# Kernel tuning notes

Hardware: AMD Instinct MI355X
Metric: run time of the kernel (lower is better)

The kernel has to match this reference:

```python
import jax, jax.numpy as jnp
import numpy as np
import math

B, N, D, H = 16, 200, 2048, 2048  # batch, seq (== max_len), feature dim, hidden/output dim


def setup_inputs() -> dict:
    key = jax.random.key(0)
    ks = jax.random.split(key, 16)
    s = 1.0 / math.sqrt(D)
    return {
        "input_query": jax.random.normal(ks[0], (B, N, D), jnp.float32),
        "input_key": jax.random.normal(ks[1], (B, N, D), jnp.float32),
        "input_value": jax.random.normal(ks[2], (B, N, D), jnp.float32),
        "loc_vector": jax.random.normal(ks[3], (B, N, D), jnp.float32),
        "Wq": jax.random.normal(ks[4], (D, H), jnp.float32) * s,
        "bq": jnp.zeros((H,), jnp.float32),
        "Wk": jax.random.normal(ks[5], (D, H), jnp.float32) * s,
        "bk": jnp.zeros((H,), jnp.float32),
        "Wv": jax.random.normal(ks[6], (D, H), jnp.float32) * s,
        "bv": jnp.zeros((H,), jnp.float32),
        "Wloc": jax.random.normal(ks[7], (D, H), jnp.float32) * s,
        "bloc": jnp.zeros((H,), jnp.float32),
        "Wlk": jax.random.normal(ks[8], (D, H), jnp.float32) * s,
        "blk": jnp.zeros((H,), jnp.float32),
        "param": jax.random.normal(ks[9], (B, N, H), jnp.float32),
    }


def reference(input_query, input_key, input_value, loc_vector,
              Wq, bq, Wk, bk, Wv, bv, Wloc, bloc, Wlk, blk, param):
    n = input_query.shape[1]
    lq = input_query @ Wq + bq                      # (b, n, h)
    lk = input_key @ Wk + bk                        # (b, m, h)
    lv = input_value @ Wv + bv                      # (b, m, o)
    loc = loc_vector[:, :n, :]
    lloc = loc @ Wloc + bloc                        # (b, n, h)
    kloc = loc @ Wlk + blk                          # (b, n, h)
    p = param[: input_query.shape[0], :n, :]        # (b, n, h)
    # Fused multi-term scores: (Q+P)K^T + (Q+Lloc)Kloc^T  == QK^T + Lloc Kloc^T + P K^T + Q Kloc^T
    scores = (jnp.einsum('bnh,bmh->bnm', lq + p, lk)
              + jnp.einsum('bnh,bmh->bnm', lq + lloc, kloc))
    attn = jax.nn.softmax(scores / math.sqrt(lq.shape[-1]), axis=-1)
    return jnp.einsum('bnm,bmo->bno', attn, lv)     # (b, n, o); dropout is identity in eval
```

## Files before the change

### kernel.cpp

```cpp
#include <hip/hip_runtime.h>
#include <hip/hip_bf16.h>
#include <math.h>

typedef float floatx4 __attribute__((ext_vector_type(4)));
typedef __bf16 bf16x8 __attribute__((ext_vector_type(8)));
typedef unsigned short ushort_t;

__device__ __forceinline__ ushort_t f2bf(float f) {
    union { float f; unsigned int i; } v; v.f = f;
    unsigned int i = v.i;
    return (ushort_t)((i + 0x7FFFu + ((i >> 16) & 1u)) >> 16);
}
__device__ __forceinline__ unsigned int pack2(float a, float b) {
    return (unsigned int)f2bf(a) | ((unsigned int)f2bf(b) << 16);
}
__device__ __forceinline__ floatx4 mfma16(bf16x8 a, bf16x8 b, floatx4 c) {
    return __builtin_amdgcn_mfma_f32_16x16x32_bf16(a, b, c, 0, 0, 0);
}
__device__ __forceinline__ void load_lds16(const ushort_t* g, ushort_t* l) {
    __builtin_amdgcn_global_load_lds(
        (const __attribute__((address_space(1))) unsigned int*)g,
        (__attribute__((address_space(3))) unsigned int*)l, 16, 0, 0);
}

__global__ __launch_bounds__(256) void k_convert(const float* __restrict__ q, const float* __restrict__ k,
                          const float* __restrict__ v, const float* __restrict__ loc,
                          ushort_t* qb, ushort_t* kb, ushort_t* vb, ushort_t* locb) {
    int z = blockIdx.y;
    const float* src = z == 0 ? q : z == 1 ? k : z == 2 ? v : loc;
    ushort_t* dst    = z == 0 ? qb : z == 1 ? kb : z == 2 ? vb : locb;
    size_t idx = (size_t)blockIdx.x * 256 + threadIdx.x;
    floatx4 f = *(const floatx4*)(src + idx * 4);
    uint2 o;
    o.x = pack2(f[0], f[1]);
    o.y = pack2(f[2], f[3]);
    *(uint2*)(dst + idx * 4) = o;
}

__global__ void k_wtrans(const float* __restrict__ w0, const float* __restrict__ w1,
                         const float* __restrict__ w2, const float* __restrict__ w3,
                         const float* __restrict__ w4,
                         ushort_t* t0, ushort_t* t1, ushort_t* t2, ushort_t* t3, ushort_t* t4) {
    __shared__ float tile[32][33];
    int z = blockIdx.z;
    const float* W = z == 0 ? w0 : z == 1 ? w1 : z == 2 ? w2 : z == 3 ? w3 : w4;
    ushort_t* T    = z == 0 ? t0 : z == 1 ? t1 : z == 2 ? t2 : z == 3 ? t3 : t4;
    int n0 = blockIdx.x * 32, k0 = blockIdx.y * 32;
    int tx = threadIdx.x & 31, ty = threadIdx.x >> 5;
#pragma unroll
    for (int i = 0; i < 4; i++) {
        int row = ty + i * 8;
        tile[row][tx] = W[(size_t)(k0 + row) * 2048 + n0 + tx];
    }
    __syncthreads();
#pragma unroll
    for (int i = 0; i < 4; i++) {
        int row = ty + i * 8;
        T[(size_t)(n0 + row) * 2048 + k0 + tx] = f2bf(tile[tx][row]);
    }
}

__global__ void k_vtrans(const ushort_t* __restrict__ lv, ushort_t* __restrict__ lvT) {
    __shared__ ushort_t tile[32][33];
    int n0 = blockIdx.x * 32;
    int t0 = blockIdx.y * 32;
    int b = blockIdx.z;
    int tx = threadIdx.x & 31, ty = threadIdx.x >> 5;
#pragma unroll
    for (int i = 0; i < 4; i++) {
        int row = ty + i * 8;
        int tk = t0 + row;
        ushort_t v = 0;
        if (tk < 200) v = lv[(size_t)(b * 200 + tk) * 2048 + n0 + tx];
        tile[row][tx] = v;
    }
    __syncthreads();
#pragma unroll
    for (int i = 0; i < 4; i++) {
        int row = ty + i * 8;
        lvT[((size_t)b * 2048 + n0 + row) * 224 + t0 + tx] = tile[tx][row];
    }
}

#define G_SB   __builtin_amdgcn_sched_barrier(0)
#define G_BAR  __builtin_amdgcn_s_barrier()
#define WVM8   asm volatile("s_waitcnt vmcnt(8)" ::: "memory")
#define WVM0   asm volatile("s_waitcnt vmcnt(0)" ::: "memory")

__global__ __launch_bounds__(256, 2) void k_gemm(
    const ushort_t* A0, const ushort_t* A1, const ushort_t* A2, const ushort_t* A3, const ushort_t* A4,
    const ushort_t* W0, const ushort_t* W1, const ushort_t* W2, const ushort_t* W3, const ushort_t* W4,
    const float* B0, const float* B1, const float* B2, const float* B3, const float* B4,
    ushort_t* lqp, ushort_t* lvp, ushort_t* llocp, ushort_t* kcat) {
    int bid = blockIdx.x;
    int tileid = (bid & 7) * 250 + (bid >> 3);
    int z = tileid / 400;
    int r = tileid - z * 400;
    int nt = r / 25;
    int mt = r - nt * 25;
    int m0 = mt * 128, n0 = nt * 128;

    const ushort_t* A  = z == 0 ? A0 : z == 1 ? A1 : z == 2 ? A2 : z == 3 ? A3 : A4;
    const ushort_t* Wt = z == 0 ? W0 : z == 1 ? W1 : z == 2 ? W2 : z == 3 ? W3 : W4;
    const float* bias  = z == 0 ? B0 : z == 1 ? B1 : z == 2 ? B2 : z == 3 ? B3 : B4;

    __shared__ ushort_t As[2][128 * 64];
    __shared__ ushort_t Bs[2][128 * 64];

    int tid = threadIdx.x;
    int lane = tid & 63, w = tid >> 6;
    int quad = lane >> 4, col = lane & 15;
    int wr = w >> 1, wc = w & 1;

    int sl = lane >> 3;
    int sc = ((lane & 7) ^ sl) * 8;
    const ushort_t* Ag[4]; const ushort_t* Bg[4]; int ldst[4];
#pragma unroll
    for (int u = 0; u < 4; u++) {
        int rowoff = u * 32 + w * 8;
        Ag[u] = A  + (size_t)(m0 + rowoff + sl) * 2048 + sc;
        Bg[u] = Wt + (size_t)(n0 + rowoff + sl) * 2048 + sc;
        ldst[u] = rowoff * 64;
    }

#define STG(KT, BUF) do { int kk = (KT) * 64;              \
        load_lds16(Ag[0] + kk, As[BUF] + ldst[0]);         \
        load_lds16(Ag[1] + kk, As[BUF] + ldst[1]);         \
        load_lds16(Ag[2] + kk, As[BUF] + ldst[2]);         \
        load_lds16(Ag[3] + kk, As[BUF] + ldst[3]);         \
        load_lds16(Bg[0] + kk, Bs[BUF] + ldst[0]);         \
        load_lds16(Bg[1] + kk, Bs[BUF] + ldst[1]);         \
        load_lds16(Bg[2] + kk, Bs[BUF] + ldst[2]);         \
        load_lds16(Bg[3] + kk, Bs[BUF] + ldst[3]); } while (0)

    int sw = col & 7;
    int ko0 = (quad ^ sw) * 8;
    int ko1 = ((4 | quad) ^ sw) * 8;
    int aro[4], bro[4];
#pragma unroll
    for (int mi = 0; mi < 4; mi++) aro[mi] = (wr * 64 + mi * 16 + col) * 64;
#pragma unroll
    for (int ni = 0; ni < 4; ni++) bro[ni] = (wc * 64 + ni * 16 + col) * 64;

    floatx4 acc[4][4] = {};

#define CMP(BUF) do {                                                     \
        bf16x8 af[4][2], bfr[4][2];                                       \
        _Pragma("unroll") for (int mi = 0; mi < 4; mi++) {                \
            af[mi][0] = *(const bf16x8*)&As[BUF][aro[mi] + ko0];          \
            af[mi][1] = *(const bf16x8*)&As[BUF][aro[mi] + ko1]; }        \
        _Pragma("unroll") for (int ni = 0; ni < 4; ni++) {                \
            bfr[ni][0] = *(const bf16x8*)&Bs[BUF][bro[ni] + ko0];         \
            bfr[ni][1] = *(const bf16x8*)&Bs[BUF][bro[ni] + ko1]; }       \
        __builtin_amdgcn_s_setprio(1);                                    \
        _Pragma("unroll") for (int mi = 0; mi < 4; mi++)                  \
        _Pragma("unroll") for (int ni = 0; ni < 4; ni++) {                \
            acc[mi][ni] = mfma16(af[mi][0], bfr[ni][0], acc[mi][ni]);     \
            acc[mi][ni] = mfma16(af[mi][1], bfr[ni][1], acc[mi][ni]); }   \
        __builtin_amdgcn_s_setprio(0); } while (0)

    STG(0, 0);

#pragma unroll 1
    for (int tt = 0; tt < 16; tt++) {
        int t0k = tt * 2;
        STG(t0k + 1, 1);
        WVM8;
        G_SB; G_BAR; G_SB;
        CMP(0);
        G_SB; G_BAR;
        STG((t0k + 2) & 31, 0);
        WVM8;
        G_SB; G_BAR; G_SB;
        CMP(1);
        G_SB; G_BAR;
    }
    WVM0;

    ushort_t* Cplain = z == 0 ? lqp : z == 2 ? lvp : llocp;
    int kcoff = (z == 4) ? 2048 : 0;
    bool to_kcat = (z == 1 || z == 4);
    float bvv[4];
#pragma unroll
    for (int ni = 0; ni < 4; ni++) bvv[ni] = bias[n0 + wc * 64 + ni * 16 + col];
#pragma unroll
    for (int mi = 0; mi < 4; mi++) {
#pragma unroll
        for (int r2 = 0; r2 < 4; r2++) {
            int m = m0 + wr * 64 + mi * 16 + quad * 4 + r2;
            ushort_t* crow;
            if (to_kcat) {
                int bb = m / 200, rr = m - bb * 200;
                crow = kcat + (size_t)(bb * 224 + rr) * 4096 + kcoff;
            } else {
                crow = Cplain + (size_t)m * 2048;
            }
#pragma unroll
            for (int ni = 0; ni < 4; ni++) {
                int n = n0 + wc * 64 + ni * 16 + col;
                crow[n] = f2bf(acc[mi][ni][r2] + bvv[ni]);
            }
        }
    }
#undef STG
#undef CMP
}

__global__ __launch_bounds__(256) void k_qprep(const ushort_t* __restrict__ lqp,
                                               const ushort_t* __restrict__ llocp,
                                               const float* __restrict__ param,
                                               ushort_t* __restrict__ qcat) {
    int m = blockIdx.x;
    int b = m / 200, r = m - b * 200;
    int c = threadIdx.x * 8;
    bf16x8 ql = *(const bf16x8*)(lqp + (size_t)m * 2048 + c);
    bf16x8 ll = *(const bf16x8*)(llocp + (size_t)m * 2048 + c);
    floatx4 p0 = *(const floatx4*)(param + (size_t)m * 2048 + c);
    floatx4 p1 = *(const floatx4*)(param + (size_t)m * 2048 + c + 4);
    bf16x8 q1, q2;
#pragma unroll
    for (int j = 0; j < 4; j++) {
        q1[j]     = (__bf16)((float)ql[j] + p0[j]);
        q1[j + 4] = (__bf16)((float)ql[j + 4] + p1[j]);
        q2[j]     = (__bf16)((float)ql[j] + (float)ll[j]);
        q2[j + 4] = (__bf16)((float)ql[j + 4] + (float)ll[j + 4]);
    }
    ushort_t* dst = qcat + ((size_t)(b * 224 + r)) * 4096 + c;
    *(bf16x8*)dst = q1;
    *(bf16x8*)(dst + 2048) = q2;
}

__global__ __launch_bounds__(256) void k_scores(const ushort_t* __restrict__ qcat,
                                                const ushort_t* __restrict__ kcat,
                                                float* __restrict__ part) {
    int qt = blockIdx.x;
    int b  = blockIdx.y;
    int kc = blockIdx.z;
    __shared__ ushort_t As[32 * 32];
    __shared__ ushort_t Bs[224 * 32];

    int tid = threadIdx.x;
    int lane = tid & 63, w = tid >> 6;
    int quad = lane >> 4, col = lane & 15;
    int srow = lane >> 2, scol = (lane & 3) * 8;

    const ushort_t* qbase = qcat + ((size_t)b * 224 + qt * 32) * 4096 + kc * 2048;
    const ushort_t* kbase = kcat + (size_t)b * 224 * 4096 + kc * 2048;

    const ushort_t* ssrc[4];
    ushort_t* sdst[4];
#pragma unroll
    for (int o = 0; o < 4; o++) {
        int id = w * 4 + o;
        if (id < 14) {
            ssrc[o] = kbase + (size_t)(id * 16 + srow) * 4096 + scol;
            sdst[o] = Bs + id * 512;
        } else {
            ssrc[o] = qbase + (size_t)((id - 14) * 16 + srow) * 4096 + scol;
            sdst[o] = As + (id - 14) * 512;
        }
    }

    floatx4 acc[2][4] = {};
    for (int k0 = 0; k0 < 2048; k0 += 32) {
        __syncthreads();
#pragma unroll
        for (int o = 0; o < 4; o++) load_lds16(ssrc[o] + k0, sdst[o]);
        __syncthreads();
        bf16x8 af[2];
#pragma unroll
        for (int mi = 0; mi < 2; mi++) af[mi] = *(const bf16x8*)&As[(mi * 16 + col) * 32 + quad * 8];
#pragma unroll
        for (int fi = 0; fi < 4; fi++) {
            int f = w + fi * 4;
            if (f < 14) {
                bf16x8 bf = *(const bf16x8*)&Bs[(f * 16 + col) * 32 + quad * 8];
#pragma unroll
                for (int mi = 0; mi < 2; mi++) acc[mi][fi] = mfma16(af[mi], bf, acc[mi][fi]);
            }
        }
    }

    float* pbase = part + ((size_t)(kc * 16 + b) * 224 + qt * 32) * 224;
#pragma unroll
    for (int fi = 0; fi < 4; fi++) {
        int f = w + fi * 4;
        if (f < 14) {
#pragma unroll
            for (int mi = 0; mi < 2; mi++)
#pragma unroll
                for (int r = 0; r < 4; r++)
                    pbase[(mi * 16 + quad * 4 + r) * 224 + f * 16 + col] = acc[mi][fi][r];
        }
    }
}

__global__ __launch_bounds__(256) void k_softmax(const float* __restrict__ part,
                                                 ushort_t* __restrict__ attn) {
    int row = blockIdx.x * 8 + (threadIdx.x >> 5);
    int b = row / 200, r = row - b * 200;
    int p = threadIdx.x & 31;
    const float* p0 = part + ((size_t)b * 224 + r) * 224;
    const float* p1 = p0 + (size_t)16 * 224 * 224;
    const float scale = 0.022097086912079608f;
    float ev[7];
    float mx = -1e30f;
#pragma unroll
    for (int j = 0; j < 7; j++) {
        int c = p * 7 + j;
        float v = (c < 200) ? (p0[c] + p1[c]) * scale : -1e30f;
        ev[j] = v;
        mx = fmaxf(mx, v);
    }
#pragma unroll
    for (int m = 1; m < 32; m <<= 1) mx = fmaxf(mx, __shfl_xor(mx, m, 32));
    float s = 0.f;
#pragma unroll
    for (int j = 0; j < 7; j++) {
        float e = __expf(ev[j] - mx);
        ev[j] = e;
        s += e;
    }
#pragma unroll
    for (int m = 1; m < 32; m <<= 1) s += __shfl_xor(s, m, 32);
    float rs = 1.0f / s;
    ushort_t* arow = attn + (size_t)row * 224;
#pragma unroll
    for (int j = 0; j < 7; j++) {
        int c = p * 7 + j;
        arow[c] = (c < 200) ? f2bf(ev[j] * rs) : (ushort_t)0;
    }
}

__global__ __launch_bounds__(256) void k_pv(const ushort_t* __restrict__ attn,
                                            const ushort_t* __restrict__ lvT,
                                            float* __restrict__ out) {
    int nt = blockIdx.x;
    int qt = blockIdx.y;
    int b = blockIdx.z;
    int tid = threadIdx.x, lane = tid & 63, w = tid >> 6;
    int quad = lane >> 4, col = lane & 15;
    int aq = qt * 16 + col; if (aq > 199) aq = 199;
    const ushort_t* arow = attn + (size_t)(b * 200 + aq) * 224;
    int nbase = nt * 128 + w * 32;
    const ushort_t* bp0 = lvT + ((size_t)b * 2048 + nbase + col) * 224;
    const ushort_t* bp1 = lvT + ((size_t)b * 2048 + nbase + 16 + col) * 224;
    floatx4 acc[2] = {};
#pragma unroll
    for (int k0 = 0; k0 < 224; k0 += 32) {
        int ko = k0 + quad * 8;
        bf16x8 av = *(const bf16x8*)(arow + ko);
        bf16x8 b0 = *(const bf16x8*)(bp0 + ko);
        bf16x8 b1 = *(const bf16x8*)(bp1 + ko);
        acc[0] = mfma16(av, b0, acc[0]);
        acc[1] = mfma16(av, b1, acc[1]);
    }
#pragma unroll
    for (int f = 0; f < 2; f++) {
        int n = nbase + f * 16 + col;
#pragma unroll
        for (int r = 0; r < 4; r++) {
            int m = qt * 16 + quad * 4 + r;
            if (m < 200) out[(size_t)(b * 200 + m) * 2048 + n] = acc[f][r];
        }
    }
}

extern "C" void kernel_launch(void* const* d_in, const int* in_sizes, int n_in,
                              void* d_out, int out_size, void* d_ws, size_t ws_size,
                              hipStream_t stream) {
    (void)in_sizes; (void)n_in; (void)out_size; (void)ws_size;
    const float* q    = (const float*)d_in[0];
    const float* k    = (const float*)d_in[1];
    const float* v    = (const float*)d_in[2];
    const float* loc  = (const float*)d_in[3];
    const float* Wq   = (const float*)d_in[4];
    const float* bq   = (const float*)d_in[5];
    const float* Wk   = (const float*)d_in[6];
    const float* bk   = (const float*)d_in[7];
    const float* Wv   = (const float*)d_in[8];
    const float* bv   = (const float*)d_in[9];
    const float* Wloc = (const float*)d_in[10];
    const float* bloc = (const float*)d_in[11];
    const float* Wlk  = (const float*)d_in[12];
    const float* blk  = (const float*)d_in[13];
    const float* param = (const float*)d_in[14];
    float* out = (float*)d_out;

    size_t off = 0;
    auto nxt = [&](size_t bytes) {
        void* p = (char*)d_ws + off;
        off += (bytes + 255) & ~(size_t)255;
        return p;
    };
    ushort_t* wt[5];
    for (int i = 0; i < 5; i++) wt[i] = (ushort_t*)nxt(2048ull * 2048 * 2);
    ushort_t* qb    = (ushort_t*)nxt(3200ull * 2048 * 2);
    ushort_t* kb    = (ushort_t*)nxt(3200ull * 2048 * 2);
    ushort_t* vb    = (ushort_t*)nxt(3200ull * 2048 * 2);
    ushort_t* locb  = (ushort_t*)nxt(3200ull * 2048 * 2);
    ushort_t* lqp   = (ushort_t*)nxt(3200ull * 2048 * 2);
    ushort_t* llocp = (ushort_t*)nxt(3200ull * 2048 * 2);
    ushort_t* lvp   = (ushort_t*)nxt(3200ull * 2048 * 2);
    ushort_t* kcat  = (ushort_t*)nxt(16ull * 224 * 4096 * 2);
    ushort_t* lvT  = wt[0];
    ushort_t* attn = wt[0] + 16ull * 2048 * 224;
    float*    part = (float*)((char*)d_ws + 2ull * 2048 * 2048 * 2);
    ushort_t* qcat = qb;

    k_convert<<<dim3(6400, 4), 256, 0, stream>>>(q, k, v, loc, qb, kb, vb, locb);
    k_wtrans<<<dim3(64, 64, 5), 256, 0, stream>>>(Wq, Wk, Wv, Wloc, Wlk,
                                                  wt[0], wt[1], wt[2], wt[3], wt[4]);
    k_gemm<<<dim3(2000), 256, 0, stream>>>(qb, kb, vb, locb, locb,
                                           wt[0], wt[1], wt[2], wt[3], wt[4],
                                           bq, bk, bv, bloc, blk,
                                           lqp, lvp, llocp, kcat);
    k_qprep<<<dim3(3200), 256, 0, stream>>>(lqp, llocp, param, qcat);
    k_vtrans<<<dim3(64, 7, 16), 256, 0, stream>>>(lvp, lvT);
    k_scores<<<dim3(7, 16, 2), 256, 0, stream>>>(qcat, kcat, part);
    k_softmax<<<dim3(400), 256, 0, stream>>>(part, attn);
    k_pv<<<dim3(16, 13, 16), 256, 0, stream>>>(attn, lvT, out);
}
```

Measured before the change: 472.2 us.

## Pipeline scores kernel with swizzled double-buffered LDS, 4-way split-K, larger PV tiles

The scores kernel now uses a double-buffered, XOR-swizzled 64-wide K tile in LDS, loaded asynchronously with global_load_lds. It raises split-K from 2 to 4 chunks to launch 448 blocks instead of 224, and the softmax kernel now sums four partial buffers. The PV kernel computes a 32x256 tile per block instead of 16x128, so each load is reused across more MFMAs. The partial-score buffer is moved to sit right after attn to fit the larger 4-way partials. Risks are extra partial-sum traffic and higher register pressure in PV.

```diff
diff --git a/kernel.cpp b/kernel.cpp
--- a/kernel.cpp
+++ b/kernel.cpp
@@ -22,6 +22,11 @@
         (const __attribute__((address_space(1))) unsigned int*)g,
         (__attribute__((address_space(3))) unsigned int*)l, 16, 0, 0);
 }
+
+#define G_SB   __builtin_amdgcn_sched_barrier(0)
+#define G_BAR  __builtin_amdgcn_s_barrier()
+#define WVM8   asm volatile("s_waitcnt vmcnt(8)" ::: "memory")
+#define WVM0   asm volatile("s_waitcnt vmcnt(0)" ::: "memory")
 
 __global__ __launch_bounds__(256) void k_convert(const float* __restrict__ q, const float* __restrict__ k,
                           const float* __restrict__ v, const float* __restrict__ loc,
@@ -81,11 +86,6 @@
         lvT[((size_t)b * 2048 + n0 + row) * 224 + t0 + tx] = tile[tx][row];
     }
 }
-
-#define G_SB   __builtin_amdgcn_sched_barrier(0)
-#define G_BAR  __builtin_amdgcn_s_barrier()
-#define WVM8   asm volatile("s_waitcnt vmcnt(8)" ::: "memory")
-#define WVM0   asm volatile("s_waitcnt vmcnt(0)" ::: "memory")
 
 __global__ __launch_bounds__(256, 2) void k_gemm(
     const ushort_t* A0, const ushort_t* A1, const ushort_t* A2, const ushort_t* A3, const ushort_t* A4,
@@ -160,7 +160,6 @@
         __builtin_amdgcn_s_setprio(0); } while (0)
 
     STG(0, 0);
-
 #pragma unroll 1
     for (int tt = 0; tt < 16; tt++) {
         int t0k = tt * 2;
@@ -230,56 +229,79 @@
     *(bf16x8*)(dst + 2048) = q2;
 }
 
-__global__ __launch_bounds__(256) void k_scores(const ushort_t* __restrict__ qcat,
-                                                const ushort_t* __restrict__ kcat,
-                                                float* __restrict__ part) {
-    int qt = blockIdx.x;
-    int b  = blockIdx.y;
-    int kc = blockIdx.z;
-    __shared__ ushort_t As[32 * 32];
-    __shared__ ushort_t Bs[224 * 32];
+__global__ __launch_bounds__(256, 2) void k_scores(const ushort_t* __restrict__ qcat,
+                                                   const ushort_t* __restrict__ kcat,
+                                                   float* __restrict__ part) {
+    int bid = blockIdx.x;
+    int tile = (bid & 7) * 56 + (bid >> 3);
+    int qt = tile % 7;
+    int t2 = tile / 7;
+    int b  = t2 & 15;
+    int kc = t2 >> 4;
+
+    __shared__ ushort_t S[2][256 * 64];
 
     int tid = threadIdx.x;
     int lane = tid & 63, w = tid >> 6;
     int quad = lane >> 4, col = lane & 15;
-    int srow = lane >> 2, scol = (lane & 3) * 8;
-
-    const ushort_t* qbase = qcat + ((size_t)b * 224 + qt * 32) * 4096 + kc * 2048;
-    const ushort_t* kbase = kcat + (size_t)b * 224 * 4096 + kc * 2048;
-
-    const ushort_t* ssrc[4];
-    ushort_t* sdst[4];
-#pragma unroll
-    for (int o = 0; o < 4; o++) {
-        int id = w * 4 + o;
-        if (id < 14) {
-            ssrc[o] = kbase + (size_t)(id * 16 + srow) * 4096 + scol;
-            sdst[o] = Bs + id * 512;
-        } else {
-            ssrc[o] = qbase + (size_t)((id - 14) * 16 + srow) * 4096 + scol;
-            sdst[o] = As + (id - 14) * 512;
-        }
-    }
+
+    int sl = lane >> 3;
+    int sc = ((lane & 7) ^ sl) * 8;
+
+    const ushort_t* qbase = qcat + ((size_t)b * 224 + qt * 32) * 4096 + kc * 1024;
+    const ushort_t* kbase = kcat + (size_t)b * 224 * 4096 + kc * 1024;
+
+    const ushort_t* gsrc[8]; int ldst[8];
+#pragma unroll
+    for (int u = 0; u < 8; u++) {
+        int row = u * 32 + w * 8;
+        gsrc[u] = (u == 0) ? qbase + (size_t)(row + sl) * 4096 + sc
+                           : kbase + (size_t)(row - 32 + sl) * 4096 + sc;
+        ldst[u] = row * 64;
+    }
+
+#define SSTG(KT, BUF) do { int kk = (KT) * 64;                        \
+        _Pragma("unroll") for (int u = 0; u < 8; u++)                 \
+            load_lds16(gsrc[u] + kk, S[BUF] + ldst[u]); } while (0)
+
+    int sw = col & 7;
+    int ko0 = (quad ^ sw) * 8;
+    int ko1 = ((4 | quad) ^ sw) * 8;
 
     floatx4 acc[2][4] = {};
-    for (int k0 = 0; k0 < 2048; k0 += 32) {
-        __syncthreads();
-#pragma unroll
-        for (int o = 0; o < 4; o++) load_lds16(ssrc[o] + k0, sdst[o]);
-        __syncthreads();
-        bf16x8 af[2];
-#pragma unroll
-        for (int mi = 0; mi < 2; mi++) af[mi] = *(const bf16x8*)&As[(mi * 16 + col) * 32 + quad * 8];
-#pragma unroll
-        for (int fi = 0; fi < 4; fi++) {
-            int f = w + fi * 4;
-            if (f < 14) {
-                bf16x8 bf = *(const bf16x8*)&Bs[(f * 16 + col) * 32 + quad * 8];
-#pragma unroll
-                for (int mi = 0; mi < 2; mi++) acc[mi][fi] = mfma16(af[mi], bf, acc[mi][fi]);
-            }
-        }
-    }
+
+#define SCMP(BUF) do {                                                    \
+        bf16x8 af[2][2];                                                  \
+        _Pragma("unroll") for (int mi = 0; mi < 2; mi++) {                \
+            int ar = (mi * 16 + col) * 64;                                \
+            af[mi][0] = *(const bf16x8*)&S[BUF][ar + ko0];                \
+            af[mi][1] = *(const bf16x8*)&S[BUF][ar + ko1]; }              \
+        __builtin_amdgcn_s_setprio(1);                                    \
+        _Pragma("unroll") for (int fi = 0; fi < 4; fi++) {                \
+            int f = w + fi * 4;                                           \
+            if (f < 14) {                                                 \
+                int br = (32 + f * 16 + col) * 64;                        \
+                bf16x8 b0 = *(const bf16x8*)&S[BUF][br + ko0];            \
+                bf16x8 b1 = *(const bf16x8*)&S[BUF][br + ko1];            \
+                _Pragma("unroll") for (int mi = 0; mi < 2; mi++) {        \
+                    acc[mi][fi] = mfma16(af[mi][0], b0, acc[mi][fi]);     \
+                    acc[mi][fi] = mfma16(af[mi][1], b1, acc[mi][fi]); }   \
+            } }                                                           \
+        __builtin_amdgcn_s_setprio(0); } while (0)
+
+    SSTG(0, 0);
+#pragma unroll 1
+    for (int tt = 0; tt < 8; tt++) {
+        SSTG(2 * tt + 1, 1);
+        WVM8; G_SB; G_BAR; G_SB;
+        SCMP(0);
+        G_SB; G_BAR;
+        SSTG((2 * tt + 2) & 15, 0);
+        WVM8; G_SB; G_BAR; G_SB;
+        SCMP(1);
+        G_SB; G_BAR;
+    }
+    WVM0;
 
     float* pbase = part + ((size_t)(kc * 16 + b) * 224 + qt * 32) * 224;
 #pragma unroll
@@ -293,6 +315,8 @@
                     pbase[(mi * 16 + quad * 4 + r) * 224 + f * 16 + col] = acc[mi][fi][r];
         }
     }
+#undef SSTG
+#undef SCMP
 }
 
 __global__ __launch_bounds__(256) void k_softmax(const float* __restrict__ part,
@@ -301,14 +325,15 @@
     int b = row / 200, r = row - b * 200;
     int p = threadIdx.x & 31;
     const float* p0 = part + ((size_t)b * 224 + r) * 224;
-    const float* p1 = p0 + (size_t)16 * 224 * 224;
+    const size_t st = (size_t)16 * 224 * 224;
     const float scale = 0.022097086912079608f;
     float ev[7];
     float mx = -1e30f;
 #pragma unroll
     for (int j = 0; j < 7; j++) {
         int c = p * 7 + j;
-        float v = (c < 200) ? (p0[c] + p1[c]) * scale : -1e30f;
+        float v = (c < 200) ? (p0[c] + p0[c + st] + p0[c + 2 * st] + p0[c + 3 * st]) * scale
+                            : -1e30f;
         ev[j] = v;
         mx = fmaxf(mx, v);
     }
@@ -340,28 +365,43 @@
     int b = blockIdx.z;
     int tid = threadIdx.x, lane = tid & 63, w = tid >> 6;
     int quad = lane >> 4, col = lane & 15;
-    int aq = qt * 16 + col; if (aq > 199) aq = 199;
-    const ushort_t* arow = attn + (size_t)(b * 200 + aq) * 224;
-    int nbase = nt * 128 + w * 32;
-    const ushort_t* bp0 = lvT + ((size_t)b * 2048 + nbase + col) * 224;
-    const ushort_t* bp1 = lvT + ((size_t)b * 2048 + nbase + 16 + col) * 224;
-    floatx4 acc[2] = {};
+    const ushort_t* arow[2];
+#pragma unroll
+    for (int mi = 0; mi < 2; mi++) {
+        int aq = qt * 32 + mi * 16 + col; if (aq > 199) aq = 199;
+        arow[mi] = attn + (size_t)(b * 200 + aq) * 224;
+    }
+    int nbase = nt * 256 + w * 64;
+    const ushort_t* bp[4];
+#pragma unroll
+    for (int ni = 0; ni < 4; ni++)
+        bp[ni] = lvT + ((size_t)b * 2048 + nbase + ni * 16 + col) * 224;
+    floatx4 acc[2][4] = {};
 #pragma unroll
     for (int k0 = 0; k0 < 224; k0 += 32) {
         int ko = k0 + quad * 8;
-        bf16x8 av = *(const bf16x8*)(arow + ko);
-        bf16x8 b0 = *(const bf16x8*)(bp0 + ko);
-        bf16x8 b1 = *(const bf16x8*)(bp1 + ko);
-        acc[0] = mfma16(av, b0, acc[0]);
-        acc[1] = mfma16(av, b1, acc[1]);
-    }
-#pragma unroll
-    for (int f = 0; f < 2; f++) {
-        int n = nbase + f * 16 + col;
+        bf16x8 av[2];
+#pragma unroll
+        for (int mi = 0; mi < 2; mi++) av[mi] = *(const bf16x8*)(arow[mi] + ko);
+#pragma unroll
+        for (int ni = 0; ni < 4; ni++) {
+            bf16x8 bv = *(const bf16x8*)(bp[ni] + ko);
+#pragma unroll
+            for (int mi = 0; mi < 2; mi++) acc[mi][ni] = mfma16(av[mi], bv, acc[mi][ni]);
+        }
+    }
+#pragma unroll
+    for (int mi = 0; mi < 2; mi++) {
 #pragma unroll
         for (int r = 0; r < 4; r++) {
-            int m = qt * 16 + quad * 4 + r;
-            if (m < 200) out[(size_t)(b * 200 + m) * 2048 + n] = acc[f][r];
+            int m = qt * 32 + mi * 16 + quad * 4 + r;
+            if (m < 200) {
+#pragma unroll
+                for (int ni = 0; ni < 4; ni++) {
+                    int n = nbase + ni * 16 + col;
+                    out[(size_t)(b * 200 + m) * 2048 + n] = acc[mi][ni][r];
+                }
+            }
         }
     }
 }
@@ -405,7 +445,7 @@
     ushort_t* kcat  = (ushort_t*)nxt(16ull * 224 * 4096 * 2);
     ushort_t* lvT  = wt[0];
     ushort_t* attn = wt[0] + 16ull * 2048 * 224;
-    float*    part = (float*)((char*)d_ws + 2ull * 2048 * 2048 * 2);
+    float*    part = (float*)(attn + 3200ull * 224);
     ushort_t* qcat = qb;
 
     k_convert<<<dim3(6400, 4), 256, 0, stream>>>(q, k, v, loc, qb, kb, vb, locb);
@@ -417,7 +457,7 @@
                                            lqp, lvp, llocp, kcat);
     k_qprep<<<dim3(3200), 256, 0, stream>>>(lqp, llocp, param, qcat);
     k_vtrans<<<dim3(64, 7, 16), 256, 0, stream>>>(lvp, lvT);
-    k_scores<<<dim3(7, 16, 2), 256, 0, stream>>>(qcat, kcat, part);
+    k_scores<<<dim3(448), 256, 0, stream>>>(qcat, kcat, part);
     k_softmax<<<dim3(400), 256, 0, stream>>>(part, attn);
-    k_pv<<<dim3(16, 13, 16), 256, 0, stream>>>(attn, lvT, out);
-}
+    k_pv<<<dim3(8, 7, 16), 256, 0, stream>>>(attn, lvT, out);
+}
```

Result: faster. 432.1 us (-8.5%).
